# Performance work log

Measured on AMD Instinct MI355X. Metric: run time of the kernel, lower is better.

Reference implementation:

```python
import jax, jax.numpy as jnp
import numpy as np

B, IN_F, OUT_F = 4096, 4096, 11008  # tokens, in_features, out_features


def setup_inputs() -> dict:
    key = jax.random.key(0)
    k1, k2, k3, k4 = jax.random.split(key, 4)
    x = jax.random.normal(k1, (B, IN_F), dtype=jnp.float32)
    # Each int holds two packed 4-bit codes (low nibble = even col, high nibble = odd col).
    packed_weights = jax.random.randint(k2, (OUT_F, IN_F // 2), 0, 256, dtype=jnp.int32)
    scales = jax.random.uniform(k3, (OUT_F,), dtype=jnp.float32) * 0.02 + 1e-4
    zero_points = jax.random.uniform(k4, (OUT_F,), dtype=jnp.float32) * 15.0
    return {"x": x, "packed_weights": packed_weights, "scales": scales,
            "zero_points": zero_points}


def _dequantize(packed_weights, scales, zero_points):
    # Unpack two 4-bit codes per byte -> q: [OUT_F, IN_F]
    low = (packed_weights & 15).astype(jnp.float32)
    high = ((packed_weights >> 4) & 15).astype(jnp.float32)
    q = jnp.stack([low, high], axis=-1).reshape(packed_weights.shape[0], -1)
    # Per-row affine dequant: w = (q - zero_point) * scale
    return (q - zero_points[:, None]) * scales[:, None]


def reference(x, packed_weights, scales, zero_points):
    W = _dequantize(packed_weights, scales, zero_points)  # [OUT_F, IN_F]
    return x @ W.T  # [B, OUT_F]
```

## Files before the change

kernel.cpp:

```cpp
#include <hip/hip_runtime.h>
#include <hip/hip_bf16.h>
#include <stdint.h>

#define M_DIM 4096
#define N_DIM 11008
#define K_DIM 4096
#define KP    (K_DIM / 2)

typedef __attribute__((ext_vector_type(4))) int i32x4;

#define AS1 __attribute__((address_space(1)))
#define AS3 __attribute__((address_space(3)))

__global__ __launch_bounds__(256) void prep(const float* __restrict__ x,
                                            const int* __restrict__ pw,
                                            signed char* __restrict__ xq,
                                            signed char* __restrict__ wq,
                                            float* __restrict__ r,
                                            float* __restrict__ sx) {
  const int b = blockIdx.x;
  const int t = threadIdx.x;
  if (b < 4096) {
    const int row = b;
    const int lane = t & 63, wid = t >> 6;
    const float4* x4 = (const float4*)(x + (size_t)row * K_DIM);
    float4 v[4];
    float am = 0.0f, sm = 0.0f;
#pragma unroll
    for (int i = 0; i < 4; ++i) {
      v[i] = x4[i * 256 + t];
      sm += v[i].x + v[i].y + v[i].z + v[i].w;
      am = fmaxf(am, fmaxf(fmaxf(fabsf(v[i].x), fabsf(v[i].y)),
                           fmaxf(fabsf(v[i].z), fabsf(v[i].w))));
    }
#pragma unroll
    for (int off = 32; off >= 1; off >>= 1) {
      am = fmaxf(am, __shfl_xor(am, off));
      sm += __shfl_xor(sm, off);
    }
    __shared__ float smax[4], ssum[4];
    if (lane == 0) { smax[wid] = am; ssum[wid] = sm; }
    __syncthreads();
    am = fmaxf(fmaxf(smax[0], smax[1]), fmaxf(smax[2], smax[3]));
    sm = ssum[0] + ssum[1] + ssum[2] + ssum[3];
    const float inv = am > 0.0f ? 127.0f / am : 0.0f;
    unsigned int* xo = (unsigned int*)(xq + (size_t)row * K_DIM);
#pragma unroll
    for (int i = 0; i < 4; ++i) {
      int q0 = min(127, max(-127, __float2int_rn(v[i].x * inv)));
      int q1 = min(127, max(-127, __float2int_rn(v[i].y * inv)));
      int q2 = min(127, max(-127, __float2int_rn(v[i].z * inv)));
      int q3 = min(127, max(-127, __float2int_rn(v[i].w * inv)));
      xo[i * 256 + t] = ((unsigned int)q0 & 0xFF) | (((unsigned int)q1 & 0xFF) << 8) |
                        (((unsigned int)q2 & 0xFF) << 16) | (((unsigned int)q3 & 0xFF) << 24);
    }
    if (t == 0) { r[row] = sm; sx[row] = am > 0.0f ? am / 127.0f : 0.0f; }
  } else {
    const int total = (N_DIM * KP) / 4;
    for (int i = (b - 4096) * 256 + t; i < total; i += 4096 * 256) {
      int4 p = ((const int4*)pw)[i];
      int v[4] = {p.x, p.y, p.z, p.w};
      unsigned int u0 = 0, u1 = 0;
#pragma unroll
      for (int j = 0; j < 2; ++j) {
        unsigned int b0 = (unsigned int)(2 * (v[j] & 15) - 15) & 0xFF;
        unsigned int b1 = (unsigned int)(2 * ((v[j] >> 4) & 15) - 15) & 0xFF;
        u0 |= (b0 | (b1 << 8)) << (16 * j);
      }
#pragma unroll
      for (int j = 0; j < 2; ++j) {
        unsigned int b0 = (unsigned int)(2 * (v[2 + j] & 15) - 15) & 0xFF;
        unsigned int b1 = (unsigned int)(2 * ((v[2 + j] >> 4) & 15) - 15) & 0xFF;
        u1 |= (b0 | (b1 << 8)) << (16 * j);
      }
      uint2 st; st.x = u0; st.y = u1;
      ((uint2*)wq)[i] = st;
    }
  }
}

#define BM 256
#define BN 256
#define BK 128
#define NTILE (K_DIM / BK)
#define NT_M (M_DIM / BM)
#define NT_N (N_DIM / BN)
#define NWG  (NT_M * NT_N)
#define HS 16384
#define PS 65536

#define WAITV(n) asm volatile("s_waitcnt vmcnt(" #n ")" ::: "memory")
#define WAITL0   asm volatile("s_waitcnt lgkmcnt(0)" ::: "memory")
#define BARR     do { asm volatile("" ::: "memory"); __builtin_amdgcn_s_barrier(); asm volatile("" ::: "memory"); } while (0)
#define SCHED0   __builtin_amdgcn_sched_barrier(0)

__global__ __launch_bounds__(512, 2) void gemm_i8(const signed char* __restrict__ Xq,
                                                  const signed char* __restrict__ Wq,
                                                  const float* __restrict__ sc,
                                                  const float* __restrict__ zp,
                                                  const float* __restrict__ rbuf,
                                                  const float* __restrict__ sxbuf,
                                                  float* __restrict__ C) {
  __shared__ __align__(16) unsigned char lds8[131072];

  const int t = threadIdx.x;
  const int bid = blockIdx.x;
  const int swz = (bid & 7) * (NWG / 8) + (bid >> 3);
  const int tm = swz & 15;
  const int tn = swz >> 4;

  const int srow = t >> 3;
  const int g0 = (t & 7) ^ (srow & 7);
  const int koff = g0 * 16;
  const signed char* pB0c0 = Wq + (size_t)(tn * BN + srow) * K_DIM + koff;
  const signed char* pB0c1 = Wq + (size_t)(tn * BN + 64 + srow) * K_DIM + koff;
  const signed char* pB1c0 = Wq + (size_t)(tn * BN + 128 + srow) * K_DIM + koff;
  const signed char* pB1c1 = Wq + (size_t)(tn * BN + 192 + srow) * K_DIM + koff;
  const signed char* pA0c0 = Xq + (size_t)(tm * BM + srow) * K_DIM + koff;
  const signed char* pA0c1 = Xq + (size_t)(tm * BM + 64 + srow) * K_DIM + koff;
  const signed char* pA1c0 = Xq + (size_t)(tm * BM + 128 + srow) * K_DIM + koff;
  const signed char* pA1c1 = Xq + (size_t)(tm * BM + 192 + srow) * K_DIM + koff;
  const int d0 = t * 16;
  const int d1 = d0 + 8192;

  const int lane = t & 63;
  const int w = t >> 6;
  const int wm = w >> 2;
  const int wn = w & 3;
  const int lr = lane & 15, lk = lane >> 4;

  const int j0 = lk ^ (lr & 7);
  const int aB0 = (2 + wm) * HS + lr * 128 + j0 * 16;
  const int aB1 = aB0 ^ 64;
  const int bB0 = (wn >> 1) * HS + (wn & 1) * 8192 + lr * 128 + j0 * 16;
  const int bB1 = bB0 ^ 64;

  i32x4 acc[8][4] = {};

#define GLL(src, dstoff) \
  __builtin_amdgcn_global_load_lds((const AS1 void*)(src), (AS3 void*)(lds8 + (dstoff)), 16, 0, 0)

  GLL(pB0c0, 0 * HS + d0); GLL(pB0c1, 0 * HS + d1);
  GLL(pB1c0, 1 * HS + d0); GLL(pB1c1, 1 * HS + d1);
  GLL(pA0c0, 2 * HS + d0); GLL(pA0c1, 2 * HS + d1);
  GLL(pA1c0, 3 * HS + d0); GLL(pA1c1, 3 * HS + d1);
  GLL(pB0c0 + BK, 4 * HS + d0); GLL(pB0c1 + BK, 4 * HS + d1);
  GLL(pB1c0 + BK, 5 * HS + d0); GLL(pB1c1 + BK, 5 * HS + d1);
  pB0c0 += 2 * BK; pB0c1 += 2 * BK; pB1c0 += 2 * BK; pB1c1 += 2 * BK;
  pA0c0 += BK;     pA0c1 += BK;     pA1c0 += BK;     pA1c1 += BK;
  WAITV(4);
  BARR;

#define TILE(P, SA, SB, VMODE) do {                                                        \
    i32x4 a0[4], a1[4], a2[4], a3[4], b0[4], b1[4];                                        \
                  \
    _Pragma("unroll") for (int i = 0; i < 4; ++i)                                          \
      a0[i] = *(const i32x4*)(lds8 + (P) * PS + aB0 + i * 2048);                           \
    _Pragma("unroll") for (int n = 0; n < 4; ++n)                                          \
      b0[n] = *(const i32x4*)(lds8 + (P) * PS + bB0 + n * 2048);                           \
    _Pragma("unroll") for (int i = 0; i < 4; ++i)                                          \
      a1[i] = *(const i32x4*)(lds8 + (P) * PS + aB0 + (4 + i) * 2048);                     \
    if (SA) { GLL(pA0c0, (((P) ^ 1) * 4 + 2) * HS + d0);                                   \
              GLL(pA0c1, (((P) ^ 1) * 4 + 2) * HS + d1);                                   \
              pA0c0 += BK; pA0c1 += BK; }                                                  \
    SCHED0;                                                                                \
    _Pragma("unroll") for (int i = 0; i < 4; ++i)                                          \
      _Pragma("unroll") for (int n = 0; n < 4; ++n)                                        \
        acc[i][n] = __builtin_amdgcn_mfma_i32_16x16x64_i8(a0[i], b0[n], acc[i][n], 0, 0, 0); \
     \
    _Pragma("unroll") for (int n = 0; n < 4; ++n)                                          \
      b1[n] = *(const i32x4*)(lds8 + (P) * PS + bB1 + n * 2048);                           \
    _Pragma("unroll") for (int i = 0; i < 4; ++i)                                          \
      a2[i] = *(const i32x4*)(lds8 + (P) * PS + aB1 + i * 2048);                           \
    if (SA) { GLL(pA1c0, (((P) ^ 1) * 4 + 3) * HS + d0);                                   \
              GLL(pA1c1, (((P) ^ 1) * 4 + 3) * HS + d1);                                   \
              pA1c0 += BK; pA1c1 += BK; }                                                  \
    SCHED0;                                                                                \
    _Pragma("unroll") for (int i = 0; i < 4; ++i)                                          \
      _Pragma("unroll") for (int n = 0; n < 4; ++n)                                        \
        acc[4 + i][n] = __builtin_amdgcn_mfma_i32_16x16x64_i8(a1[i], b0[n], acc[4 + i][n], 0, 0, 0); \
    WAITL0;                                                                                \
    BARR;                                                                                  \
                            \
    _Pragma("unroll") for (int i = 0; i < 4; ++i)                                          \
      a3[i] = *(const i32x4*)(lds8 + (P) * PS + aB1 + (4 + i) * 2048);                     \
    if (SB) { GLL(pB0c0, ((P) * 4 + 0) * HS + d0);                                         \
              GLL(pB0c1, ((P) * 4 + 0) * HS + d1);                                         \
              pB0c0 += BK; pB0c1 += BK; }                                                  \
    SCHED0;                                                                                \
    _Pragma("unroll") for (int i = 0; i < 4; ++i)                                          \
      _Pragma("unroll") for (int n = 0; n < 4; ++n)                                        \
        acc[i][n] = __builtin_amdgcn_mfma_i32_16x16x64_i8(a2[i], b1[n], acc[i][n], 0, 0, 0); \
                        \
    if (SB) { GLL(pB1c0, ((P) * 4 + 1) * HS + d0);                                         \
              GLL(pB1c1, ((P) * 4 + 1) * HS + d1);                                         \
              pB1c0 += BK; pB1c1 += BK; }                                                  \
    SCHED0;                                                                                \
    _Pragma("unroll") for (int i = 0; i < 4; ++i)                                          \
      _Pragma("unroll") for (int n = 0; n < 4; ++n)                                        \
        acc[4 + i][n] = __builtin_amdgcn_mfma_i32_16x16x64_i8(a3[i], b1[n], acc[4 + i][n], 0, 0, 0); \
    if ((VMODE) == 0) { WAITV(4); } else if ((VMODE) == 1) { WAITV(0); }                   \
    BARR;                                                                                  \
  } while (0)

  for (int it = 0; it < (NTILE - 2) / 2; ++it) {
    TILE(0, 1, 1, 0);
    TILE(1, 1, 1, 0);
  }
  TILE(0, 1, 0, 1);
  TILE(1, 0, 0, 2);

#undef TILE
#undef GLL

  const int row0 = tm * BM + wm * 128 + lk * 4;
  const int col0 = tn * BN + wn * 64 + lr;
  float sv[4], zv[4];
#pragma unroll
  for (int n = 0; n < 4; ++n) {
    sv[n] = sc[col0 + n * 16];
    zv[n] = 7.5f - zp[col0 + n * 16];
  }
#pragma unroll
  for (int m = 0; m < 8; ++m)
#pragma unroll
    for (int rr = 0; rr < 4; ++rr) {
      const int row = row0 + m * 16 + rr;
      const float rv = rbuf[row];
      const float hx = 0.5f * sxbuf[row];
#pragma unroll
      for (int n = 0; n < 4; ++n)
        C[(size_t)row * N_DIM + col0 + n * 16] = sv[n] * (hx * (float)acc[m][n][rr] + zv[n] * rv);
    }
}

__global__ __launch_bounds__(256) void fallback_gemm(const float* __restrict__ x,
                                                     const int* __restrict__ pw,
                                                     const float* __restrict__ sc,
                                                     const float* __restrict__ zp,
                                                     float* __restrict__ out) {
  __shared__ float Xs[64][33];
  __shared__ float Ws[64][33];
  const int bid = blockIdx.x;
  const int bm = bid & 63;
  const int bn = bid >> 6;
  const int t = threadIdx.x;
  const int tx = t & 15, ty = t >> 4;
  float acc[4][4] = {};
  for (int k0 = 0; k0 < K_DIM; k0 += 32) {
    __syncthreads();
#pragma unroll
    for (int i = 0; i < 8; ++i) {
      int e = t + i * 256; int rr = e >> 5, c = e & 31;
      Xs[rr][c] = x[(size_t)(bm * 64 + rr) * K_DIM + k0 + c];
    }
#pragma unroll
    for (int i = 0; i < 4; ++i) {
      int e = t + i * 256; int rr = e >> 4, jj = e & 15;
      int row = bn * 64 + rr;
      int v = pw[(size_t)row * KP + (k0 >> 1) + jj];
      float s = sc[row], z = zp[row];
      Ws[rr][2 * jj]     = ((float)(v & 15) - z) * s;
      Ws[rr][2 * jj + 1] = ((float)((v >> 4) & 15) - z) * s;
    }
    __syncthreads();
#pragma unroll
    for (int kk = 0; kk < 32; ++kk) {
      float a[4], b[4];
#pragma unroll
      for (int i2 = 0; i2 < 4; ++i2) a[i2] = Xs[ty * 4 + i2][kk];
#pragma unroll
      for (int j2 = 0; j2 < 4; ++j2) b[j2] = Ws[tx * 4 + j2][kk];
#pragma unroll
      for (int i2 = 0; i2 < 4; ++i2)
#pragma unroll
        for (int j2 = 0; j2 < 4; ++j2) acc[i2][j2] += a[i2] * b[j2];
    }
  }
#pragma unroll
  for (int i2 = 0; i2 < 4; ++i2)
#pragma unroll
    for (int j2 = 0; j2 < 4; ++j2)
      out[(size_t)(bm * 64 + ty * 4 + i2) * N_DIM + bn * 64 + tx * 4 + j2] = acc[i2][j2];
}

extern "C" void kernel_launch(void* const* d_in, const int* in_sizes, int n_in,
                              void* d_out, int out_size, void* d_ws, size_t ws_size,
                              hipStream_t stream) {
  const float* x  = (const float*)d_in[0];
  const int*   pw = (const int*)d_in[1];
  const float* sc = (const float*)d_in[2];
  const float* zp = (const float*)d_in[3];
  float* out = (float*)d_out;

  const size_t wq_b = (size_t)N_DIM * K_DIM;
  const size_t xq_b = (size_t)M_DIM * K_DIM;
  const size_t need = wq_b + xq_b + 2 * 4096 * sizeof(float);

  if (ws_size >= need) {
    signed char* wq = (signed char*)d_ws;
    signed char* xq = wq + wq_b;
    float* rbuf  = (float*)((char*)d_ws + wq_b + xq_b);
    float* sxbuf = rbuf + 4096;
    hipLaunchKernelGGL(prep,    dim3(4096 + 4096), dim3(256), 0, stream, x, pw, xq, wq, rbuf, sxbuf);
    hipLaunchKernelGGL(gemm_i8, dim3(NWG),         dim3(512), 0, stream, xq, wq, sc, zp, rbuf, sxbuf, out);
  } else {
    hipLaunchKernelGGL(fallback_gemm, dim3(64 * 172), dim3(256), 0, stream, x, pw, sc, zp, out);
  }
}
```

Baseline: 216.3 us.

## Triple-buffer B tiles in LDS to drop the mid-tile barrier

```diff
diff --git a/kernel.cpp b/kernel.cpp
--- a/kernel.cpp
+++ b/kernel.cpp
@@ -87,10 +87,10 @@
 #define NT_N (N_DIM / BN)
 #define NWG  (NT_M * NT_N)
 #define HS 16384
-#define PS 65536
+#define BPAR 32768
+#define ABASE 98304
 
 #define WAITV(n) asm volatile("s_waitcnt vmcnt(" #n ")" ::: "memory")
-#define WAITL0   asm volatile("s_waitcnt lgkmcnt(0)" ::: "memory")
 #define BARR     do { asm volatile("" ::: "memory"); __builtin_amdgcn_s_barrier(); asm volatile("" ::: "memory"); } while (0)
 #define SCHED0   __builtin_amdgcn_sched_barrier(0)
 
@@ -101,7 +101,7 @@
                                                   const float* __restrict__ rbuf,
                                                   const float* __restrict__ sxbuf,
                                                   float* __restrict__ C) {
-  __shared__ __align__(16) unsigned char lds8[131072];
+  __shared__ __align__(16) unsigned char lds8[163840];
 
   const int t = threadIdx.x;
   const int bid = blockIdx.x;
@@ -130,70 +130,66 @@
   const int lr = lane & 15, lk = lane >> 4;
 
   const int j0 = lk ^ (lr & 7);
-  const int aB0 = (2 + wm) * HS + lr * 128 + j0 * 16;
-  const int aB1 = aB0 ^ 64;
+  const int aB0 = ABASE + wm * HS + lr * 128 + j0 * 16;
   const int bB0 = (wn >> 1) * HS + (wn & 1) * 8192 + lr * 128 + j0 * 16;
-  const int bB1 = bB0 ^ 64;
 
   i32x4 acc[8][4] = {};
 
 #define GLL(src, dstoff) \
   __builtin_amdgcn_global_load_lds((const AS1 void*)(src), (AS3 void*)(lds8 + (dstoff)), 16, 0, 0)
 
-  GLL(pB0c0, 0 * HS + d0); GLL(pB0c1, 0 * HS + d1);
-  GLL(pB1c0, 1 * HS + d0); GLL(pB1c1, 1 * HS + d1);
-  GLL(pA0c0, 2 * HS + d0); GLL(pA0c1, 2 * HS + d1);
-  GLL(pA1c0, 3 * HS + d0); GLL(pA1c1, 3 * HS + d1);
-  GLL(pB0c0 + BK, 4 * HS + d0); GLL(pB0c1 + BK, 4 * HS + d1);
-  GLL(pB1c0 + BK, 5 * HS + d0); GLL(pB1c1 + BK, 5 * HS + d1);
+  GLL(pB0c0, 0 * BPAR + d0);          GLL(pB0c1, 0 * BPAR + d1);
+  GLL(pB1c0, 0 * BPAR + HS + d0);     GLL(pB1c1, 0 * BPAR + HS + d1);
+  GLL(pA0c0, ABASE + d0);             GLL(pA0c1, ABASE + d1);
+  GLL(pA1c0, ABASE + HS + d0);        GLL(pA1c1, ABASE + HS + d1);
+  GLL(pB0c0 + BK, 1 * BPAR + d0);     GLL(pB0c1 + BK, 1 * BPAR + d1);
+  GLL(pB1c0 + BK, 1 * BPAR + HS + d0);GLL(pB1c1 + BK, 1 * BPAR + HS + d1);
   pB0c0 += 2 * BK; pB0c1 += 2 * BK; pB1c0 += 2 * BK; pB1c1 += 2 * BK;
   pA0c0 += BK;     pA0c1 += BK;     pA1c0 += BK;     pA1c1 += BK;
   WAITV(4);
   BARR;
 
-#define TILE(P, SA, SB, VMODE) do {                                                        \
+#define TILE(PB, PA, SA, SB, VMODE) do {                                                   \
     i32x4 a0[4], a1[4], a2[4], a3[4], b0[4], b1[4];                                        \
                   \
     _Pragma("unroll") for (int i = 0; i < 4; ++i)                                          \
-      a0[i] = *(const i32x4*)(lds8 + (P) * PS + aB0 + i * 2048);                           \
+      a0[i] = *(const i32x4*)(lds8 + (PA) * BPAR + aB0 + i * 2048);                        \
     _Pragma("unroll") for (int n = 0; n < 4; ++n)                                          \
-      b0[n] = *(const i32x4*)(lds8 + (P) * PS + bB0 + n * 2048);                           \
-    _Pragma("unroll") for (int i = 0; i < 4; ++i)                                          \
-      a1[i] = *(const i32x4*)(lds8 + (P) * PS + aB0 + (4 + i) * 2048);                     \
-    if (SA) { GLL(pA0c0, (((P) ^ 1) * 4 + 2) * HS + d0);                                   \
-              GLL(pA0c1, (((P) ^ 1) * 4 + 2) * HS + d1);                                   \
+      b0[n] = *(const i32x4*)(lds8 + (PB) * BPAR + bB0 + n * 2048);                        \
+    _Pragma("unroll") for (int i = 0; i < 4; ++i)                                          \
+      a1[i] = *(const i32x4*)(lds8 + (PA) * BPAR + aB0 + (4 + i) * 2048);                  \
+    if (SA) { GLL(pA0c0, ABASE + ((PA) ^ 1) * BPAR + d0);                                  \
+              GLL(pA0c1, ABASE + ((PA) ^ 1) * BPAR + d1);                                  \
               pA0c0 += BK; pA0c1 += BK; }                                                  \
     SCHED0;                                                                                \
     _Pragma("unroll") for (int i = 0; i < 4; ++i)                                          \
       _Pragma("unroll") for (int n = 0; n < 4; ++n)                                        \
         acc[i][n] = __builtin_amdgcn_mfma_i32_16x16x64_i8(a0[i], b0[n], acc[i][n], 0, 0, 0); \
-     \
+              \
     _Pragma("unroll") for (int n = 0; n < 4; ++n)                                          \
-      b1[n] = *(const i32x4*)(lds8 + (P) * PS + bB1 + n * 2048);                           \
-    _Pragma("unroll") for (int i = 0; i < 4; ++i)                                          \
-      a2[i] = *(const i32x4*)(lds8 + (P) * PS + aB1 + i * 2048);                           \
-    if (SA) { GLL(pA1c0, (((P) ^ 1) * 4 + 3) * HS + d0);                                   \
-              GLL(pA1c1, (((P) ^ 1) * 4 + 3) * HS + d1);                                   \
+      b1[n] = *(const i32x4*)(lds8 + (PB) * BPAR + (bB0 ^ 64) + n * 2048);                 \
+    _Pragma("unroll") for (int i = 0; i < 4; ++i)                                          \
+      a2[i] = *(const i32x4*)(lds8 + (PA) * BPAR + (aB0 ^ 64) + i * 2048);                 \
+    if (SA) { GLL(pA1c0, ABASE + ((PA) ^ 1) * BPAR + HS + d0);                             \
+              GLL(pA1c1, ABASE + ((PA) ^ 1) * BPAR + HS + d1);                             \
               pA1c0 += BK; pA1c1 += BK; }                                                  \
     SCHED0;                                                                                \
     _Pragma("unroll") for (int i = 0; i < 4; ++i)                                          \
       _Pragma("unroll") for (int n = 0; n < 4; ++n)                                        \
         acc[4 + i][n] = __builtin_amdgcn_mfma_i32_16x16x64_i8(a1[i], b0[n], acc[4 + i][n], 0, 0, 0); \
-    WAITL0;                                                                                \
-    BARR;                                                                                  \
-                            \
-    _Pragma("unroll") for (int i = 0; i < 4; ++i)                                          \
-      a3[i] = *(const i32x4*)(lds8 + (P) * PS + aB1 + (4 + i) * 2048);                     \
-    if (SB) { GLL(pB0c0, ((P) * 4 + 0) * HS + d0);                                         \
-              GLL(pB0c1, ((P) * 4 + 0) * HS + d1);                                         \
+         \
+    _Pragma("unroll") for (int i = 0; i < 4; ++i)                                          \
+      a3[i] = *(const i32x4*)(lds8 + (PA) * BPAR + (aB0 ^ 64) + (4 + i) * 2048);           \
+    if (SB) { GLL(pB0c0, (((PB) + 2) % 3) * BPAR + d0);                                    \
+              GLL(pB0c1, (((PB) + 2) % 3) * BPAR + d1);                                    \
               pB0c0 += BK; pB0c1 += BK; }                                                  \
     SCHED0;                                                                                \
     _Pragma("unroll") for (int i = 0; i < 4; ++i)                                          \
       _Pragma("unroll") for (int n = 0; n < 4; ++n)                                        \
         acc[i][n] = __builtin_amdgcn_mfma_i32_16x16x64_i8(a2[i], b1[n], acc[i][n], 0, 0, 0); \
-                        \
-    if (SB) { GLL(pB1c0, ((P) * 4 + 1) * HS + d0);                                         \
-              GLL(pB1c1, ((P) * 4 + 1) * HS + d1);                                         \
+                          \
+    if (SB) { GLL(pB1c0, (((PB) + 2) % 3) * BPAR + HS + d0);                               \
+              GLL(pB1c1, (((PB) + 2) % 3) * BPAR + HS + d1);                               \
               pB1c0 += BK; pB1c1 += BK; }                                                  \
     SCHED0;                                                                                \
     _Pragma("unroll") for (int i = 0; i < 4; ++i)                                          \
@@ -203,12 +199,16 @@
     BARR;                                                                                  \
   } while (0)
 
-  for (int it = 0; it < (NTILE - 2) / 2; ++it) {
-    TILE(0, 1, 1, 0);
-    TILE(1, 1, 1, 0);
-  }
-  TILE(0, 1, 0, 1);
-  TILE(1, 0, 0, 2);
+  for (int it = 0; it < 5; ++it) {
+    TILE(0, 0, 1, 1, 0);
+    TILE(1, 1, 1, 1, 0);
+    TILE(2, 0, 1, 1, 0);
+    TILE(0, 1, 1, 1, 0);
+    TILE(1, 0, 1, 1, 0);
+    TILE(2, 1, 1, 1, 0);
+  }
+  TILE(0, 0, 1, 0, 1);
+  TILE(1, 1, 0, 0, 2);
 
 #undef TILE
 #undef GLL
```

After: 216.7 us. No clear change (+0.2%).
